# Kernel optimization log

Hardware: AMD Instinct MI355X
Metric: run time of the kernel (lower is better)

## Reference

```python
import jax, jax.numpy as jnp
import numpy as np

B, S, D = 2, 2048, 1024
H, DK, DV = 16, 64, 64
EPS = 1e-5
SQRT_DK = float(np.sqrt(DK))


def setup_inputs() -> dict:
    key = jax.random.key(0)
    ks = jax.random.split(key, 8)
    sc = 0.02
    return {
        "x": jax.random.normal(ks[0], (B, S, D), jnp.float32),
        "Wk": jax.random.normal(ks[1], (D, H * DK), jnp.float32) * sc,
        "bk": jnp.zeros((H * DK,), jnp.float32),
        "Wq": jax.random.normal(ks[2], (D, H * DK), jnp.float32) * sc,
        "bq": jnp.zeros((H * DK,), jnp.float32),
        "Wv": jax.random.normal(ks[3], (D, H * DV), jnp.float32) * sc,
        "bv": jnp.zeros((H * DV,), jnp.float32),
        "Wo": jax.random.normal(ks[4], (H * DV, D), jnp.float32) * sc,
        "bo": jnp.zeros((D,), jnp.float32),
        "gamma": jnp.ones((D,), jnp.float32),
        "beta": jnp.zeros((D,), jnp.float32),
    }


def reference(x, Wk, bk, Wq, bq, Wv, bv, Wo, bo, gamma, beta):
    b, s, d = x.shape
    # NOTE: original torch code reshapes (B, S, H*dk) directly to (B, H, S, dk)
    # without a transpose; we replicate that exact (non-standard) reshape.
    keys = (x @ Wk + bk).reshape(b, H, s, DK)
    queries = (x @ Wq + bq).reshape(b, H, s, DK)
    values = (x @ Wv + bv).reshape(b, H, s, DV)

    scores = jnp.einsum('bhqd,bhkd->bhqk', queries, keys) / SQRT_DK
    causal_mask = jnp.triu(jnp.ones((s, s), bool), k=1)  # True = masked
    scores = jnp.where(causal_mask[None, None], jnp.float32(-1e9), scores)
    attention = jax.nn.softmax(scores, axis=-1)

    context = jnp.einsum('bhqk,bhkd->bhqd', attention, values)
    context = context.reshape(b, s, H * DV)

    out = context @ Wo + bo  # dropout is identity at inference
    out = out + x            # residual connection

    mean = jnp.mean(out, axis=-1, keepdims=True)
    var = jnp.mean(jnp.square(out - mean), axis=-1, keepdims=True)
    return (out - mean) / jnp.sqrt(var + EPS) * gamma + beta
```

## Files before the change

### kernel.cpp

```cpp
#include <hip/hip_runtime.h>


typedef __attribute__((ext_vector_type(8))) __bf16 bf16x8;
typedef __attribute__((ext_vector_type(8))) unsigned short ushort8;
typedef __attribute__((ext_vector_type(4))) unsigned short u16x4;
typedef __attribute__((ext_vector_type(4))) float f32x4;
typedef __attribute__((ext_vector_type(4))) unsigned int u32x4;

static __device__ __forceinline__ unsigned short f2bf(float f) {
    unsigned u = __builtin_bit_cast(unsigned, f);
    u += 0x7fffu + ((u >> 16) & 1u);
    return (unsigned short)(u >> 16);
}

static __device__ __forceinline__ float bf2f(unsigned short u) {
    return __builtin_bit_cast(float, (unsigned)u << 16);
}

static __device__ __forceinline__ unsigned cvt_pk_bf16(float lo, float hi) {
    unsigned r;
    asm("v_cvt_pk_bf16_f32 %0, %1, %2" : "=v"(r) : "v"(lo), "v"(hi));
    return r;
}

__global__ __launch_bounds__(256) void prep_kernel(
    const float* __restrict__ x,
    const float* __restrict__ Wq, const float* __restrict__ Wk,
    const float* __restrict__ Wv, const float* __restrict__ Wo,
    unsigned short* __restrict__ xb, unsigned short* __restrict__ WT)
{
    const int tid = threadIdx.x;
    const int z = blockIdx.z;
    if (z == 4) {
        const int bid = blockIdx.y * 16 + blockIdx.x;
        const int base = bid * 4096 + tid;
        #pragma unroll
        for (int it = 0; it < 16; it++) {
            int i = base + it * 256;
            float4 v = ((const float4*)x)[i];
            ushort4 o;
            o.x = f2bf(v.x); o.y = f2bf(v.y); o.z = f2bf(v.z); o.w = f2bf(v.w);
            ((ushort4*)xb)[i] = o;
        }
        return;
    }
    const float* src = (z == 0) ? Wq : (z == 1) ? Wk : (z == 2) ? Wv : Wo;
    unsigned short* dst = WT + ((size_t)z << 20);
    __shared__ __align__(16) unsigned short t[64 * 68];
    const int n0 = blockIdx.x * 64, k0 = blockIdx.y * 64;
    #pragma unroll
    for (int u = 0; u < 4; u++) {
        int e = u * 256 + tid;
        int r = e >> 4, c4 = (e & 15) * 4;
        float4 v = *(const float4*)(src + (k0 + r) * 1024 + n0 + c4);
        ushort4 o;
        o.x = f2bf(v.x); o.y = f2bf(v.y); o.z = f2bf(v.z); o.w = f2bf(v.w);
        *(ushort4*)(t + r * 68 + c4) = o;
    }
    __syncthreads();
    #pragma unroll
    for (int u = 0; u < 4; u++) {
        int e = u * 256 + tid;
        int rn = e >> 4, ck = (e & 15) * 4;
        ushort4 o;
        o.x = t[(ck + 0) * 68 + rn];
        o.y = t[(ck + 1) * 68 + rn];
        o.z = t[(ck + 2) * 68 + rn];
        o.w = t[(ck + 3) * 68 + rn];
        *(ushort4*)(dst + (n0 + rn) * 1024 + k0 + ck) = o;
    }
}

__global__ __launch_bounds__(256) void vtrans_kernel(const unsigned short* __restrict__ V,
                                                     unsigned short* __restrict__ VT) {
    __shared__ __align__(16) unsigned short t[64 * 68];
    const int tid = threadIdx.x;
    const int p0 = blockIdx.x * 64;
    const long base = (long)blockIdx.y * 131072;
    #pragma unroll
    for (int u = 0; u < 2; u++) {
        int e = u * 256 + tid;
        int r = e >> 3, c8 = (e & 7) * 8;
        ushort8 v = *(const ushort8*)(V + base + (long)(p0 + r) * 64 + c8);
        *(ushort8*)(t + r * 68 + c8) = v;
    }
    __syncthreads();
    #pragma unroll
    for (int u = 0; u < 4; u++) {
        int e = u * 256 + tid;
        int dv = e >> 4, pk = (e & 15) * 4;
        ushort4 o;
        o.x = t[(pk + 0) * 68 + dv];
        o.y = t[(pk + 1) * 68 + dv];
        o.z = t[(pk + 2) * 68 + dv];
        o.w = t[(pk + 3) * 68 + dv];
        *(ushort4*)(VT + base + (long)dv * 2048 + p0 + pk) = o;
    }
}

__global__ __launch_bounds__(256, 3) void gemm_kernel(
    const unsigned short* __restrict__ A,
    const unsigned short* __restrict__ Bt,
    const float* __restrict__ b0, const float* __restrict__ b1, const float* __restrict__ b2,
    unsigned short* __restrict__ outQ, unsigned short* __restrict__ outK,
    unsigned short* __restrict__ outV,
    const float* __restrict__ resid, int mode)
{
    __shared__ __align__(16) unsigned short As[2][128 * 32];
    __shared__ __align__(16) unsigned short Bs[2][128 * 32];
    const int tid = threadIdx.x;
    const int lane = tid & 63, wave = tid >> 6;
    const int quad = lane >> 4, l16 = lane & 15;
    const int wm = wave >> 1, wn = wave & 1;
    const int row0 = blockIdx.y * 128, n0g = blockIdx.x * 128;

    const int sr = tid >> 2;
    const int sc = (tid & 3) * 8;
    const unsigned short* Ag0 = A + (size_t)(row0 + sr) * 1024 + sc;
    const unsigned short* Ag1 = A + (size_t)(row0 + 64 + sr) * 1024 + sc;
    const unsigned short* Bg0 = Bt + (size_t)(n0g + sr) * 1024 + sc;
    const unsigned short* Bg1 = Bt + (size_t)(n0g + 64 + sr) * 1024 + sc;

    {
        ushort8 a0 = *(const ushort8*)(Ag0);
        ushort8 a1 = *(const ushort8*)(Ag1);
        ushort8 bv0 = *(const ushort8*)(Bg0);
        ushort8 bv1 = *(const ushort8*)(Bg1);
        *(ushort8*)(As[0] + sr * 32 + sc) = a0;
        *(ushort8*)(As[0] + (64 + sr) * 32 + sc) = a1;
        *(ushort8*)(Bs[0] + sr * 32 + sc) = bv0;
        *(ushort8*)(Bs[0] + (64 + sr) * 32 + sc) = bv1;
    }
    __syncthreads();

    f32x4 acc[4][4] = {};
    #pragma unroll 2
    for (int it = 0; it < 32; ++it) {
        const int cur = it & 1;
        ushort8 na0, na1, nb0, nb1;
        if (it < 31) {
            const int k0 = (it + 1) * 32;
            na0 = *(const ushort8*)(Ag0 + k0);
            na1 = *(const ushort8*)(Ag1 + k0);
            nb0 = *(const ushort8*)(Bg0 + k0);
            nb1 = *(const ushort8*)(Bg1 + k0);
        }
        bf16x8 af[4], bfr[4];
        #pragma unroll
        for (int i = 0; i < 4; i++)
            af[i] = *(const bf16x8*)(As[cur] + (wm * 64 + i * 16 + l16) * 32 + quad * 8);
        #pragma unroll
        for (int j = 0; j < 4; j++)
            bfr[j] = *(const bf16x8*)(Bs[cur] + (wn * 64 + j * 16 + l16) * 32 + quad * 8);
        #pragma unroll
        for (int i = 0; i < 4; i++)
            #pragma unroll
            for (int j = 0; j < 4; j++)
                acc[i][j] = __builtin_amdgcn_mfma_f32_16x16x32_bf16(af[i], bfr[j], acc[i][j], 0, 0, 0);
        if (it < 31) {
            const int nxt = cur ^ 1;
            *(ushort8*)(As[nxt] + sr * 32 + sc) = na0;
            *(ushort8*)(As[nxt] + (64 + sr) * 32 + sc) = na1;
            *(ushort8*)(Bs[nxt] + sr * 32 + sc) = nb0;
            *(ushort8*)(Bs[nxt] + (64 + sr) * 32 + sc) = nb1;
            __syncthreads();
        }
    }

    if (mode == 0) {
        const int which = n0g >> 10;
        const float* bp = (which == 0) ? b0 : (which == 1) ? b1 : b2;
        unsigned short* op = (which == 0) ? outQ : (which == 1) ? outK : outV;
        const float scl = (which == 0) ? 0.125f : 1.0f;
        #pragma unroll
        for (int i = 0; i < 4; i++)
            #pragma unroll
            for (int j = 0; j < 4; j++) {
                int c = (n0g + wn * 64 + j * 16 + l16) & 1023;
                float bj = bp[c];
                #pragma unroll
                for (int r = 0; r < 4; r++) {
                    int r_g = row0 + wm * 64 + i * 16 + quad * 4 + r;
                    op[(size_t)r_g * 1024 + c] = f2bf((acc[i][j][r] + bj) * scl);
                }
            }
    } else {
        #pragma unroll
        for (int i = 0; i < 4; i++)
            #pragma unroll
            for (int j = 0; j < 4; j++) {
                int c_g = n0g + wn * 64 + j * 16 + l16;
                float bj = b0[c_g];
                #pragma unroll
                for (int r = 0; r < 4; r++) {
                    int r_g = row0 + wm * 64 + i * 16 + quad * 4 + r;
                    size_t idx = (size_t)r_g * 1024 + c_g;
                    outQ[idx] = f2bf(acc[i][j][r] + bj + resid[idx]);
                }
            }
    }
}

__global__ __launch_bounds__(256, 4) void flash_kernel(
    const unsigned short* __restrict__ Q,
    const unsigned short* __restrict__ K,
    const unsigned short* __restrict__ VT,
    unsigned short* __restrict__ Ctx)
{
    __shared__ __align__(16) unsigned short Kt[128 * 72];
    __shared__ __align__(16) unsigned short Vt[64 * 136];
    const int tid = threadIdx.x;
    const int lane = tid & 63, wave = tid >> 6;
    const int quad = lane >> 4, l16 = lane & 15;
    const int qb = 31 - blockIdx.y;
    const int q0 = qb * 64;
    const long base = (long)blockIdx.x * 131072;
    const int nt = (qb + 2) >> 1;

    bf16x8 qa[2];
    #pragma unroll
    for (int h = 0; h < 2; h++)
        qa[h] = *(const bf16x8*)(Q + base + (q0 + wave * 16 + l16) * 64 + h * 32 + quad * 8);

    f32x4 o[4] = {};
    float l_one = 0.f;
    const int qpos = q0 + wave * 16 + l16;

    #pragma unroll
    for (int u = 0; u < 4; u++) {
        int e = u * 256 + tid;
        int r = e >> 3, c = (e & 7) * 8;
        *(ushort8*)(Kt + r * 72 + c) = *(const ushort8*)(K + base + (long)r * 64 + c);
        int dv = e >> 4, kc = (e & 15) * 8;
        *(ushort8*)(Vt + dv * 136 + kc) = *(const ushort8*)(VT + base + (long)dv * 2048 + kc);
    }
    __syncthreads();

    for (int t = 0; t < nt; t++) {
        ushort8 nk[4], nv[4];
        if (t + 1 < nt) {
            const int k1 = (t + 1) * 128;
            #pragma unroll
            for (int u = 0; u < 4; u++) {
                int e = u * 256 + tid;
                int r = e >> 3, c = (e & 7) * 8;
                nk[u] = *(const ushort8*)(K + base + (long)(k1 + r) * 64 + c);
                int dv = e >> 4, kc = (e & 15) * 8;
                nv[u] = *(const ushort8*)(VT + base + (long)dv * 2048 + k1 + kc);
            }
        }
        const int k0 = t * 128;
        const bool diag = (t == nt - 1);
        const int kkmax = diag ? ((q0 - k0 + wave * 16 + 15) >> 5) : 3;

        #pragma unroll
        for (int kk = 0; kk < 4; kk++) {
            if (kk <= kkmax) {
                const int cE = kk * 2, cO = kk * 2 + 1;
                f32x4 aE = {}, aO = {};
                {
                    bf16x8 kb0 = *(const bf16x8*)(Kt + (cE * 16 + l16) * 72 + quad * 8);
                    bf16x8 kb1 = *(const bf16x8*)(Kt + (cE * 16 + l16) * 72 + 32 + quad * 8);
                    aE = __builtin_amdgcn_mfma_f32_16x16x32_bf16(kb0, qa[0], aE, 0, 0, 0);
                    aE = __builtin_amdgcn_mfma_f32_16x16x32_bf16(kb1, qa[1], aE, 0, 0, 0);
                }
                {
                    bf16x8 kb0 = *(const bf16x8*)(Kt + (cO * 16 + l16) * 72 + quad * 8);
                    bf16x8 kb1 = *(const bf16x8*)(Kt + (cO * 16 + l16) * 72 + 32 + quad * 8);
                    aO = __builtin_amdgcn_mfma_f32_16x16x32_bf16(kb0, qa[0], aO, 0, 0, 0);
                    aO = __builtin_amdgcn_mfma_f32_16x16x32_bf16(kb1, qa[1], aO, 0, 0, 0);
                }
                float pE[4], pO[4];
                #pragma unroll
                for (int r = 0; r < 4; r++) {
                    float e1 = __expf(aE[r]);
                    float e2 = __expf(aO[r]);
                    if (diag) {
                        int kE = k0 + cE * 16 + quad * 4 + r;
                        int kO = k0 + cO * 16 + quad * 4 + r;
                        e1 = (kE > qpos) ? 0.f : e1;
                        e2 = (kO > qpos) ? 0.f : e2;
                    }
                    pE[r] = e1; pO[r] = e2;
                }
                l_one += (pE[0] + pE[1]) + (pE[2] + pE[3])
                       + (pO[0] + pO[1]) + (pO[2] + pO[3]);
                unsigned w0 = cvt_pk_bf16(pE[0], pE[1]);
                unsigned w1 = cvt_pk_bf16(pE[2], pE[3]);
                unsigned w2 = cvt_pk_bf16(pO[0], pO[1]);
                unsigned w3 = cvt_pk_bf16(pO[2], pO[3]);
                asm("v_permlane32_swap_b32 %0, %1" : "+v"(w0), "+v"(w2));
                asm("v_permlane16_swap_b32 %0, %1" : "+v"(w0), "+v"(w2));
                asm("v_permlane32_swap_b32 %0, %1" : "+v"(w1), "+v"(w3));
                asm("v_permlane16_swap_b32 %0, %1" : "+v"(w1), "+v"(w3));
                u32x4 pu;
                pu[0] = w0; pu[1] = w1; pu[2] = w2; pu[3] = w3;
                bf16x8 pa = __builtin_bit_cast(bf16x8, pu);
                #pragma unroll
                for (int c2 = 0; c2 < 4; c2++) {
                    bf16x8 vb = *(const bf16x8*)(Vt + (c2 * 16 + l16) * 136 + kk * 32 + quad * 8);
                    o[c2] = __builtin_amdgcn_mfma_f32_16x16x32_bf16(pa, vb, o[c2], 0, 0, 0);
                }
            }
        }
        __syncthreads();
        if (t + 1 < nt) {
            #pragma unroll
            for (int u = 0; u < 4; u++) {
                int e = u * 256 + tid;
                int r = e >> 3, c = (e & 7) * 8;
                *(ushort8*)(Kt + r * 72 + c) = nk[u];
                int dv = e >> 4, kc = (e & 15) * 8;
                *(ushort8*)(Vt + dv * 136 + kc) = nv[u];
            }
            __syncthreads();
        }
    }

    l_one += __shfl_xor(l_one, 16, 64);
    l_one += __shfl_xor(l_one, 32, 64);
    float rinv[4];
    #pragma unroll
    for (int r = 0; r < 4; r++)
        rinv[r] = 1.0f / __shfl(l_one, quad * 4 + r, 16);
    #pragma unroll
    for (int c2 = 0; c2 < 4; c2++)
        #pragma unroll
        for (int r = 0; r < 4; r++) {
            int row = q0 + wave * 16 + quad * 4 + r;
            Ctx[base + (long)row * 64 + c2 * 16 + l16] = f2bf(o[c2][r] * rinv[r]);
        }
}

__global__ __launch_bounds__(256) void ln_kernel(const unsigned short* __restrict__ inp,
                                                 const float* __restrict__ gamma,
                                                 const float* __restrict__ beta,
                                                 float* __restrict__ out)
{
    __shared__ float ssum[4], ssq[4];
    const int row = blockIdx.x;
    const int tid = threadIdx.x;
    ushort4 uv = ((const ushort4*)(inp + (size_t)row * 1024))[tid];
    float vx = bf2f(uv.x), vy = bf2f(uv.y), vz = bf2f(uv.z), vw = bf2f(uv.w);
    float s = vx + vy + vz + vw;
    float q = vx * vx + vy * vy + vz * vz + vw * vw;
    #pragma unroll
    for (int off = 32; off >= 1; off >>= 1) {
        s += __shfl_xor(s, off, 64);
        q += __shfl_xor(q, off, 64);
    }
    if ((tid & 63) == 0) { ssum[tid >> 6] = s; ssq[tid >> 6] = q; }
    __syncthreads();
    float ts = ssum[0] + ssum[1] + ssum[2] + ssum[3];
    float tq = ssq[0] + ssq[1] + ssq[2] + ssq[3];
    float mean = ts * (1.f / 1024.f);
    float var = tq * (1.f / 1024.f) - mean * mean;
    float rinv = rsqrtf(var + 1e-5f);
    float4 g = ((const float4*)gamma)[tid];
    float4 b = ((const float4*)beta)[tid];
    float4 o;
    o.x = (vx - mean) * rinv * g.x + b.x;
    o.y = (vy - mean) * rinv * g.y + b.y;
    o.z = (vz - mean) * rinv * g.z + b.z;
    o.w = (vw - mean) * rinv * g.w + b.w;
    ((float4*)(out + (size_t)row * 1024))[tid] = o;
}

extern "C" void kernel_launch(void* const* d_in, const int* in_sizes, int n_in,
                              void* d_out, int out_size, void* d_ws, size_t ws_size,
                              hipStream_t stream) {
    const float* x     = (const float*)d_in[0];
    const float* Wk    = (const float*)d_in[1];
    const float* bk    = (const float*)d_in[2];
    const float* Wq    = (const float*)d_in[3];
    const float* bq    = (const float*)d_in[4];
    const float* Wv    = (const float*)d_in[5];
    const float* bv    = (const float*)d_in[6];
    const float* Wo    = (const float*)d_in[7];
    const float* bo    = (const float*)d_in[8];
    const float* gamma = (const float*)d_in[9];
    const float* beta  = (const float*)d_in[10];
    float* out = (float*)d_out;

    char* ws = (char*)d_ws;
    unsigned short* xb    = (unsigned short*)(ws);
    unsigned short* WqkvT = (unsigned short*)(ws + (8ull << 20));
    unsigned short* Qb    = (unsigned short*)(ws + (16ull << 20));
    unsigned short* Kb    = (unsigned short*)(ws + (24ull << 20));
    unsigned short* VbT   = (unsigned short*)(ws + (32ull << 20));
    unsigned short* Cb    = (unsigned short*)(ws + (40ull << 20));
    unsigned short* outp  = (unsigned short*)(ws + (48ull << 20));
    unsigned short* WoT   = WqkvT + (3u << 20);
    unsigned short* Vbn   = Cb;

    dim3 pgrid(16, 16, 5);
    prep_kernel<<<pgrid, 256, 0, stream>>>(x, Wq, Wk, Wv, Wo, xb, WqkvT);

    dim3 qkvgrid(24, 32);
    gemm_kernel<<<qkvgrid, 256, 0, stream>>>(xb, WqkvT, bq, bk, bv,
                                             Qb, Kb, Vbn, nullptr, 0);

    dim3 vgrid(32, 32);
    vtrans_kernel<<<vgrid, 256, 0, stream>>>(Vbn, VbT);

    dim3 fgrid(32, 32);
    flash_kernel<<<fgrid, 256, 0, stream>>>(Qb, Kb, VbT, Cb);

    dim3 ogrid(8, 32);
    gemm_kernel<<<ogrid, 256, 0, stream>>>(Cb, WoT, bo, nullptr, nullptr,
                                           outp, nullptr, nullptr, x, 1);

    ln_kernel<<<4096, 256, 0, stream>>>(outp, gamma, beta, out);
}
```

Before: 202.7 us.

## Read K directly from global, drop permlane swaps, and interleave query-block order

The K tile is no longer staged through shared memory; each wave loads its K fragments straight from global memory (relying on cache), which cuts LDS traffic and the K store before each barrier. The permlane swaps on the P fragment are replaced by reading V in two 4-element halves, so the MFMA operand layouts still line up. Query blocks are also remapped so heavy and light causal blocks alternate for better load balance. The risks are higher global/L2 latency inside the inner loop and less efficient 8-byte LDS reads for V.

New measurement: 229.9 us. +13.4%, slower.

```diff
diff --git a/kernel.cpp b/kernel.cpp
--- a/kernel.cpp
+++ b/kernel.cpp
@@ -207,12 +207,13 @@
     const unsigned short* __restrict__ VT,
     unsigned short* __restrict__ Ctx)
 {
-    __shared__ __align__(16) unsigned short Kt[128 * 72];
     __shared__ __align__(16) unsigned short Vt[64 * 136];
     const int tid = threadIdx.x;
     const int lane = tid & 63, wave = tid >> 6;
     const int quad = lane >> 4, l16 = lane & 15;
-    const int qb = 31 - blockIdx.y;
+    const int y = blockIdx.y;
+    const int qb = (y < 8) ? (31 - y) : (y < 16) ? (y - 8)
+                 : (y < 24) ? (39 - y) : (y - 16);
     const int q0 = qb * 64;
     const long base = (long)blockIdx.x * 131072;
     const int nt = (qb + 2) >> 1;
@@ -225,26 +226,23 @@
     f32x4 o[4] = {};
     float l_one = 0.f;
     const int qpos = q0 + wave * 16 + l16;
+    const unsigned short* Kp = K + base;
 
     #pragma unroll
     for (int u = 0; u < 4; u++) {
         int e = u * 256 + tid;
-        int r = e >> 3, c = (e & 7) * 8;
-        *(ushort8*)(Kt + r * 72 + c) = *(const ushort8*)(K + base + (long)r * 64 + c);
         int dv = e >> 4, kc = (e & 15) * 8;
         *(ushort8*)(Vt + dv * 136 + kc) = *(const ushort8*)(VT + base + (long)dv * 2048 + kc);
     }
     __syncthreads();
 
     for (int t = 0; t < nt; t++) {
-        ushort8 nk[4], nv[4];
+        ushort8 nv[4];
         if (t + 1 < nt) {
             const int k1 = (t + 1) * 128;
             #pragma unroll
             for (int u = 0; u < 4; u++) {
                 int e = u * 256 + tid;
-                int r = e >> 3, c = (e & 7) * 8;
-                nk[u] = *(const ushort8*)(K + base + (long)(k1 + r) * 64 + c);
                 int dv = e >> 4, kc = (e & 15) * 8;
                 nv[u] = *(const ushort8*)(VT + base + (long)dv * 2048 + k1 + kc);
             }
@@ -259,14 +257,16 @@
                 const int cE = kk * 2, cO = kk * 2 + 1;
                 f32x4 aE = {}, aO = {};
                 {
-                    bf16x8 kb0 = *(const bf16x8*)(Kt + (cE * 16 + l16) * 72 + quad * 8);
-                    bf16x8 kb1 = *(const bf16x8*)(Kt + (cE * 16 + l16) * 72 + 32 + quad * 8);
+                    const unsigned short* kr = Kp + (k0 + cE * 16 + l16) * 64 + quad * 8;
+                    bf16x8 kb0 = *(const bf16x8*)(kr);
+                    bf16x8 kb1 = *(const bf16x8*)(kr + 32);
                     aE = __builtin_amdgcn_mfma_f32_16x16x32_bf16(kb0, qa[0], aE, 0, 0, 0);
                     aE = __builtin_amdgcn_mfma_f32_16x16x32_bf16(kb1, qa[1], aE, 0, 0, 0);
                 }
                 {
-                    bf16x8 kb0 = *(const bf16x8*)(Kt + (cO * 16 + l16) * 72 + quad * 8);
-                    bf16x8 kb1 = *(const bf16x8*)(Kt + (cO * 16 + l16) * 72 + 32 + quad * 8);
+                    const unsigned short* kr = Kp + (k0 + cO * 16 + l16) * 64 + quad * 8;
+                    bf16x8 kb0 = *(const bf16x8*)(kr);
+                    bf16x8 kb1 = *(const bf16x8*)(kr + 32);
                     aO = __builtin_amdgcn_mfma_f32_16x16x32_bf16(kb0, qa[0], aO, 0, 0, 0);
                     aO = __builtin_amdgcn_mfma_f32_16x16x32_bf16(kb1, qa[1], aO, 0, 0, 0);
                 }
@@ -285,20 +285,21 @@
                 }
                 l_one += (pE[0] + pE[1]) + (pE[2] + pE[3])
                        + (pO[0] + pO[1]) + (pO[2] + pO[3]);
-                unsigned w0 = cvt_pk_bf16(pE[0], pE[1]);
-                unsigned w1 = cvt_pk_bf16(pE[2], pE[3]);
-                unsigned w2 = cvt_pk_bf16(pO[0], pO[1]);
-                unsigned w3 = cvt_pk_bf16(pO[2], pO[3]);
-                asm("v_permlane32_swap_b32 %0, %1" : "+v"(w0), "+v"(w2));
-                asm("v_permlane16_swap_b32 %0, %1" : "+v"(w0), "+v"(w2));
-                asm("v_permlane32_swap_b32 %0, %1" : "+v"(w1), "+v"(w3));
-                asm("v_permlane16_swap_b32 %0, %1" : "+v"(w1), "+v"(w3));
                 u32x4 pu;
-                pu[0] = w0; pu[1] = w1; pu[2] = w2; pu[3] = w3;
+                pu[0] = cvt_pk_bf16(pE[0], pE[1]);
+                pu[1] = cvt_pk_bf16(pE[2], pE[3]);
+                pu[2] = cvt_pk_bf16(pO[0], pO[1]);
+                pu[3] = cvt_pk_bf16(pO[2], pO[3]);
                 bf16x8 pa = __builtin_bit_cast(bf16x8, pu);
                 #pragma unroll
                 for (int c2 = 0; c2 < 4; c2++) {
-                    bf16x8 vb = *(const bf16x8*)(Vt + (c2 * 16 + l16) * 136 + kk * 32 + quad * 8);
+                    const unsigned short* vr = Vt + (c2 * 16 + l16) * 136 + kk * 32 + quad * 4;
+                    u16x4 v0 = *(const u16x4*)(vr);
+                    u16x4 v1 = *(const u16x4*)(vr + 16);
+                    ushort8 vv;
+                    vv[0] = v0[0]; vv[1] = v0[1]; vv[2] = v0[2]; vv[3] = v0[3];
+                    vv[4] = v1[0]; vv[5] = v1[1]; vv[6] = v1[2]; vv[7] = v1[3];
+                    bf16x8 vb = __builtin_bit_cast(bf16x8, vv);
                     o[c2] = __builtin_amdgcn_mfma_f32_16x16x32_bf16(pa, vb, o[c2], 0, 0, 0);
                 }
             }
@@ -308,8 +309,6 @@
             #pragma unroll
             for (int u = 0; u < 4; u++) {
                 int e = u * 256 + tid;
-                int r = e >> 3, c = (e & 7) * 8;
-                *(ushort8*)(Kt + r * 72 + c) = nk[u];
                 int dv = e >> 4, kc = (e & 15) * 8;
                 *(ushort8*)(Vt + dv * 136 + kc) = nv[u];
             }
```
